# Kernel tuning notes

Measured on AMD Instinct MI355X. Metric: run time of the kernel, lower is better.

The kernel has to match this reference:

```python
import jax, jax.numpy as jnp
import numpy as np

B, T, I, H, O = 32, 2048, 128, 256, 64


def setup_inputs() -> dict:
    key = jax.random.key(0)
    ks = jax.random.split(key, 7)
    s = 0.05
    return {
        "x": jax.random.normal(ks[0], (B, T, I), dtype=jnp.float32),
        # PyTorch LSTM params (single layer): gate order i, f, g, o
        "W_ih": jax.random.normal(ks[1], (4 * H, I), dtype=jnp.float32) * s,
        "W_hh": jax.random.normal(ks[2], (4 * H, H), dtype=jnp.float32) * s,
        "b_ih": jax.random.normal(ks[3], (4 * H,), dtype=jnp.float32) * s,
        "b_hh": jax.random.normal(ks[4], (4 * H,), dtype=jnp.float32) * s,
        "W_fc": jax.random.normal(ks[5], (O, H), dtype=jnp.float32) * s,
        "b_fc": jax.random.normal(ks[6], (O,), dtype=jnp.float32) * s,
    }


def _lstm(x, W_ih, W_hh, b_ih, b_hh):
    # x: (B, T, I) -> hidden states (B, T, H). PyTorch gate order i,f,g,o.
    Bn, Tn, _ = x.shape
    Hn = W_hh.shape[1]
    # Precompute input projection once (memory-bound friendly):
    x_proj = jnp.einsum("bti,gi->btg", x, W_ih) + b_ih + b_hh  # (B, T, 4H)
    x_proj = jnp.swapaxes(x_proj, 0, 1)  # (T, B, 4H)

    def step(carry, xt):
        h, c = carry
        gates = xt + h @ W_hh.T  # (B, 4H)
        i, f, g, o = jnp.split(gates, 4, axis=-1)
        i = jax.nn.sigmoid(i)
        f = jax.nn.sigmoid(f)
        g = jnp.tanh(g)
        o = jax.nn.sigmoid(o)
        c = f * c + i * g
        h = o * jnp.tanh(c)
        return (h, c), h

    h0 = jnp.zeros((Bn, Hn), dtype=x.dtype)
    c0 = jnp.zeros((Bn, Hn), dtype=x.dtype)
    _, hs = jax.lax.scan(step, (h0, c0), x_proj)  # (T, B, H)
    return jnp.swapaxes(hs, 0, 1)  # (B, T, H)


def reference(x, W_ih, W_hh, b_ih, b_hh, W_fc, b_fc):
    h = _lstm(x, W_ih, W_hh, b_ih, b_hh)          # (B, T, H)
    logits = jnp.einsum("bth,oh->bto", h, W_fc) + b_fc  # fused fc over all (b,t)
    # original applies softmax over the feature vector at each (i, j)
    return jax.nn.softmax(logits, axis=-1)        # (B, T, O)
```

## Files before the change

kernel.cpp:

```cpp
#include <hip/hip_runtime.h>
#include <hip/hip_bf16.h>
#include <hip/hip_fp16.h>

typedef _Float16 v2h __attribute__((ext_vector_type(2)));

__device__ __forceinline__ float fdot2u(unsigned int a, unsigned int b, float c){
  return __builtin_amdgcn_fdot2(__builtin_bit_cast(v2h, a), __builtin_bit_cast(v2h, b), c, false);
}
__device__ __forceinline__ unsigned int packh2(float a, float b){
  union{ _Float16 h[2]; unsigned int u; } z;
  z.h[0] = (_Float16)a; z.h[1] = (_Float16)b; return z.u;
}
__device__ __forceinline__ float h2f(unsigned short s){
  return (float)__builtin_bit_cast(_Float16, s);
}
__device__ __forceinline__ float sigf(float x){
  return __builtin_amdgcn_rcpf(1.0f + __builtin_amdgcn_exp2f(-1.44269504f*x));
}
__device__ __forceinline__ float tanhf_(float x){
  return 2.0f*__builtin_amdgcn_rcpf(1.0f + __builtin_amdgcn_exp2f(-2.88539008f*x)) - 1.0f;
}

__global__ void prep_kernel(const float* __restrict__ Whh, const float* __restrict__ Wfc,
                            const float* __restrict__ bih, const float* __restrict__ bhh,
                            unsigned int* __restrict__ whhT, unsigned int* __restrict__ wfc16,
                            float* __restrict__ bsum){
  int i = blockIdx.x*256 + threadIdx.x;
  if (i < 131072){
    int r = i >> 7, d = i & 127;
    int q = d >> 2, l = d & 3;
    whhT[q*4096 + r*4 + l] = packh2(Whh[r*256 + 2*d], Whh[r*256 + 2*d + 1]);
  } else if (i < 139264){
    int j = i - 131072; int o = j >> 7, d = j & 127;
    wfc16[j] = packh2(Wfc[o*256 + 2*d], Wfc[o*256 + 2*d + 1]);
  } else if (i < 140288){
    int g = i - 139264;
    bsum[g] = bih[g] + bhh[g];
  }
}

#define XS 68
__global__ __launch_bounds__(256) void xproj_kernel(const float* __restrict__ x,
                          const float* __restrict__ Wih,
                          const float* __restrict__ bsum, unsigned int* __restrict__ xproj){
  __shared__ unsigned int lx[128*XS];
  __shared__ unsigned int lw[64*XS];
  __shared__ float lb[64];
  int t  = threadIdx.x;
  int bt0 = blockIdx.x*128, g0 = blockIdx.y*64;
  int rr = t >> 4, cc = t & 15;
  #pragma unroll
  for (int it=0; it<8; ++it){
    int row = rr + it*16;
    const float4* s = (const float4*)(x + (size_t)(bt0+row)*128 + cc*8);
    float4 a = s[0], b = s[1];
    uint4 w; w.x=packh2(a.x,a.y); w.y=packh2(a.z,a.w); w.z=packh2(b.x,b.y); w.w=packh2(b.z,b.w);
    *(uint4*)&lx[row*XS + cc*4] = w;
  }
  #pragma unroll
  for (int it=0; it<4; ++it){
    int row = rr + it*16;
    const float4* s = (const float4*)(Wih + (size_t)(g0+row)*128 + cc*8);
    float4 a = s[0], b = s[1];
    uint4 w; w.x=packh2(a.x,a.y); w.y=packh2(a.z,a.w); w.z=packh2(b.x,b.y); w.w=packh2(b.z,b.w);
    *(uint4*)&lw[row*XS + cc*4] = w;
  }
  if (t < 64) lb[t] = bsum[g0 + t];
  __syncthreads();

  float acc[8][4];
  #pragma unroll
  for (int j=0;j<8;++j)
    #pragma unroll
    for (int i=0;i<4;++i) acc[j][i]=0.f;

  #pragma unroll
  for (int d4=0; d4<16; ++d4){
    uint4 wv[4], xv[8];
    #pragma unroll
    for (int i=0;i<4;++i) wv[i] = *(const uint4*)&lw[(cc*4+i)*XS + d4*4];
    #pragma unroll
    for (int j=0;j<8;++j) xv[j] = *(const uint4*)&lx[(rr*8+j)*XS + d4*4];
    #pragma unroll
    for (int j=0;j<8;++j){
      #pragma unroll
      for (int i=0;i<4;++i){
        float a = acc[j][i];
        a = fdot2u(xv[j].x, wv[i].x, a);
        a = fdot2u(xv[j].y, wv[i].y, a);
        a = fdot2u(xv[j].z, wv[i].z, a);
        a = fdot2u(xv[j].w, wv[i].w, a);
        acc[j][i] = a;
      }
    }
  }
  #pragma unroll
  for (int j=0;j<8;++j){
    int bt = bt0 + rr*8 + j;
    uint2 o2;
    o2.x = packh2(acc[j][0]+lb[cc*4+0], acc[j][1]+lb[cc*4+1]);
    o2.y = packh2(acc[j][2]+lb[cc*4+2], acc[j][3]+lb[cc*4+3]);
    *(uint2*)&xproj[(size_t)bt*512 + (g0>>1) + cc*2] = o2;
  }
}

#define WR4 24
#define WL4 8
#define HOFF (WL4*4096)
#define GOFF (HOFF + 256)

extern "C" __global__ void __launch_bounds__(1024,4) lstm_kernel(
    const unsigned int* __restrict__ whhT, const unsigned int* __restrict__ xproj,
    unsigned short* __restrict__ h_all)
{
  extern __shared__ unsigned int lds[];
  uint4* lw4 = (uint4*)lds;
  float* gbuf = (float*)(lds + GOFF);
  const int t = threadIdx.x;
  const int g = t >> 8, u = t & 255;
  const int b = blockIdx.x;

  const uint4* wsrc = (const uint4*)whhT;
  uint4 w4[WR4];
  #pragma unroll
  for (int d=0; d<WR4; ++d) w4[d] = wsrc[d*1024 + t];
  #pragma unroll
  for (int q=0; q<WL4; ++q) lw4[q*1024 + t] = wsrc[(WR4+q)*1024 + t];
  if (t < 128) lds[HOFF + t] = 0u;

  const unsigned short* xpb = (const unsigned short*)xproj + (size_t)b*2048*1024;
  unsigned short xn = xpb[t];
  float c = 0.f;
  unsigned short* hout = h_all + (size_t)b*2048*256 + u;
  __syncthreads();

  for (int tt=0; tt<2048; ++tt){
    const int cur = tt & 1;
    float A0 = h2f(xn), A1 = 0.f;

    int tn = (tt+1 < 2048) ? tt+1 : 2047;
    xn = xpb[(size_t)tn*1024 + t];

    const unsigned int* hb = lds + HOFF + cur*128;
    #pragma unroll
    for (int d=0; d<WR4; ++d){
      uint4 h4 = *(const uint4*)(hb + d*4);
      A0 = fdot2u(w4[d].x, h4.x, A0); A1 = fdot2u(w4[d].y, h4.y, A1);
      A0 = fdot2u(w4[d].z, h4.z, A0); A1 = fdot2u(w4[d].w, h4.w, A1);
    }
    #pragma unroll
    for (int q=0; q<WL4; ++q){
      uint4 wl = lw4[q*1024 + t];
      uint4 h4 = *(const uint4*)(hb + (WR4+q)*4);
      A0 = fdot2u(wl.x, h4.x, A0); A1 = fdot2u(wl.y, h4.y, A1);
      A0 = fdot2u(wl.z, h4.z, A0); A1 = fdot2u(wl.w, h4.w, A1);
    }
    float a = A0 + A1;
    float v = (g == 2) ? tanhf_(a) : sigf(a);
    gbuf[g*256 + u] = v;
    __syncthreads();

    float gi = gbuf[u];
    float gf = gbuf[256 + u];
    float gg = gbuf[512 + u];
    float go = gbuf[768 + u];
    c = gf*c + gi*gg;
    float h = go * tanhf_(c);
    unsigned short hh = __builtin_bit_cast(unsigned short, (_Float16)h);
    if (g == 0){
      ((unsigned short*)(lds + HOFF + (cur^1)*128))[u] = hh;
      hout[(size_t)tt*256] = hh;
    }
    __syncthreads();
  }
}

__global__ __launch_bounds__(1024) void fc_softmax_kernel(const unsigned short* __restrict__ h_all,
      const unsigned int* __restrict__ wfc16, const float* __restrict__ bfc,
      float* __restrict__ out){
  __shared__ unsigned int lwf[64*132];
  __shared__ unsigned int lh[16*132];
  int t = threadIdx.x;
  int bt0 = blockIdx.x*16;
  {
    const uint4* s = (const uint4*)(wfc16 + (size_t)t*8);
    uint4 a = s[0], b = s[1];
    unsigned int* dst = &lwf[(t>>4)*132 + (t&15)*8];
    *(uint4*)dst = a; *(uint4*)(dst+4) = b;
  }
  {
    int row = t>>6, col = (t&63)*2;
    const unsigned int* hsrc = (const unsigned int*)h_all;
    uint2 v = *(const uint2*)(hsrc + (size_t)(bt0+row)*128 + col);
    *(uint2*)&lh[row*132 + col] = v;
  }
  __syncthreads();
  int w = t>>6, o = t&63;
  int bt = bt0 + w;
  float acc = bfc[o];
  #pragma unroll
  for (int d4=0; d4<32; ++d4){
    uint4 hq = *(const uint4*)&lh[w*132 + d4*4];
    uint4 wq = *(const uint4*)&lwf[o*132 + d4*4];
    acc = fdot2u(wq.x, hq.x, acc);
    acc = fdot2u(wq.y, hq.y, acc);
    acc = fdot2u(wq.z, hq.z, acc);
    acc = fdot2u(wq.w, hq.w, acc);
  }
  float m = acc;
  #pragma unroll
  for (int off=32; off>=1; off>>=1) m = fmaxf(m, __shfl_xor(m, off));
  float e = __builtin_amdgcn_exp2f(1.44269504f*(acc - m));
  float s = e;
  #pragma unroll
  for (int off=32; off>=1; off>>=1) s += __shfl_xor(s, off);
  out[(size_t)bt*64 + o] = e * __builtin_amdgcn_rcpf(s);
}

extern "C" void kernel_launch(void* const* d_in, const int* in_sizes, int n_in,
                              void* d_out, int out_size, void* d_ws, size_t ws_size,
                              hipStream_t stream){
  const float* x   = (const float*)d_in[0];
  const float* Wih = (const float*)d_in[1];
  const float* Whh = (const float*)d_in[2];
  const float* bih = (const float*)d_in[3];
  const float* bhh = (const float*)d_in[4];
  const float* Wfc = (const float*)d_in[5];
  const float* bfc = (const float*)d_in[6];
  float* out = (float*)d_out;

  char* ws = (char*)d_ws;
  unsigned int*   xproj = (unsigned int*)ws;
  unsigned short* h_all = (unsigned short*)(ws + 134217728);
  unsigned int*   whhT  = (unsigned int*)(ws + 134217728 + 33554432);
  unsigned int*   wfc16 = whhT + 131072;
  float*          bsum  = (float*)(wfc16 + 8192);

  prep_kernel<<<548, 256, 0, stream>>>(Whh, Wfc, bih, bhh, whhT, wfc16, bsum);
  dim3 gb(512, 16);
  xproj_kernel<<<gb, 256, 0, stream>>>(x, Wih, bsum, xproj);
  int dyn = (GOFF + 1024) * 4;
  hipFuncSetAttribute((const void*)lstm_kernel, hipFuncAttributeMaxDynamicSharedMemorySize, dyn);
  lstm_kernel<<<32, 1024, dyn, stream>>>(whhT, xproj, h_all);
  fc_softmax_kernel<<<4096, 1024, 0, stream>>>(h_all, wfc16, bfc, out);
}
```

Before: 3.457 ms.

## Split LSTM recurrence by hidden-dim quarter to drop one barrier per step

Each group of four consecutive threads now owns one hidden unit. Each thread holds all four gate rows over a quarter of the hidden dimension, so gate pre-activations are reduced with two xor shuffles instead of an LDS gate buffer and a second __syncthreads. The W_hh layout in prep is rearranged to match. Each thread also reads only its own padded slice of h, which cuts LDS broadcast reads. The cost is four transcendental gate evaluations per thread and replicated cell-state math, and all four lanes now write h to LDS.

```diff
diff --git a/kernel.cpp b/kernel.cpp
--- a/kernel.cpp
+++ b/kernel.cpp
@@ -23,13 +23,14 @@
 
 __global__ void prep_kernel(const float* __restrict__ Whh, const float* __restrict__ Wfc,
                             const float* __restrict__ bih, const float* __restrict__ bhh,
-                            unsigned int* __restrict__ whhT, unsigned int* __restrict__ wfc16,
+                            unsigned int* __restrict__ whhT2, unsigned int* __restrict__ wfc16,
                             float* __restrict__ bsum){
   int i = blockIdx.x*256 + threadIdx.x;
   if (i < 131072){
     int r = i >> 7, d = i & 127;
-    int q = d >> 2, l = d & 3;
-    whhT[q*4096 + r*4 + l] = packh2(Whh[r*256 + 2*d], Whh[r*256 + 2*d + 1]);
+    int g = r >> 8, u = r & 255;
+    int p = d >> 5, j = (d >> 2) & 7, l = d & 3;
+    whhT2[(size_t)((g*8+j)*1024 + u*4 + p)*4 + l] = packh2(Whh[r*256 + 2*d], Whh[r*256 + 2*d + 1]);
   } else if (i < 139264){
     int j = i - 131072; int o = j >> 7, d = j & 127;
     wfc16[j] = packh2(Wfc[o*256 + 2*d], Wfc[o*256 + 2*d + 1]);
@@ -104,73 +105,78 @@
   }
 }
 
-#define WR4 24
 #define WL4 8
 #define HOFF (WL4*4096)
-#define GOFF (HOFF + 256)
+#define HBUF 528
 
 extern "C" __global__ void __launch_bounds__(1024,4) lstm_kernel(
-    const unsigned int* __restrict__ whhT, const unsigned int* __restrict__ xproj,
+    const unsigned int* __restrict__ whhT2, const unsigned int* __restrict__ xproj,
     unsigned short* __restrict__ h_all)
 {
   extern __shared__ unsigned int lds[];
   uint4* lw4 = (uint4*)lds;
-  float* gbuf = (float*)(lds + GOFF);
+  unsigned short* lds16 = (unsigned short*)lds;
   const int t = threadIdx.x;
-  const int g = t >> 8, u = t & 255;
+  const int u = t >> 2, p = t & 3;
   const int b = blockIdx.x;
-
-  const uint4* wsrc = (const uint4*)whhT;
-  uint4 w4[WR4];
-  #pragma unroll
-  for (int d=0; d<WR4; ++d) w4[d] = wsrc[d*1024 + t];
-  #pragma unroll
-  for (int q=0; q<WL4; ++q) lw4[q*1024 + t] = wsrc[(WR4+q)*1024 + t];
-  if (t < 128) lds[HOFF + t] = 0u;
-
+  const int p164 = p*164;
+
+  const uint4* wsrc = (const uint4*)whhT2;
+  uint4 w4[3][8];
+  #pragma unroll
+  for (int g=0; g<3; ++g)
+    #pragma unroll
+    for (int j=0; j<8; ++j) w4[g][j] = wsrc[(g*8+j)*1024 + t];
+  #pragma unroll
+  for (int q=0; q<WL4; ++q) lw4[q*1024 + t] = wsrc[(24+q)*1024 + t];
+  if (t < HBUF) lds[HOFF + t] = 0u;
+
+  const float m0 = (p==0)?1.f:0.f, m1 = (p==1)?1.f:0.f,
+              m2 = (p==2)?1.f:0.f, m3 = (p==3)?1.f:0.f;
   const unsigned short* xpb = (const unsigned short*)xproj + (size_t)b*2048*1024;
-  unsigned short xn = xpb[t];
+  const int xoff = p*256 + u;
+  unsigned short xn = xpb[xoff];
   float c = 0.f;
   unsigned short* hout = h_all + (size_t)b*2048*256 + u;
   __syncthreads();
 
   for (int tt=0; tt<2048; ++tt){
     const int cur = tt & 1;
-    float A0 = h2f(xn), A1 = 0.f;
-
+    float A0 = 0.f, A1 = 0.f, A2 = 0.f, A3 = 0.f;
+    float xv = h2f(xn);
     int tn = (tt+1 < 2048) ? tt+1 : 2047;
-    xn = xpb[(size_t)tn*1024 + t];
-
-    const unsigned int* hb = lds + HOFF + cur*128;
-    #pragma unroll
-    for (int d=0; d<WR4; ++d){
-      uint4 h4 = *(const uint4*)(hb + d*4);
-      A0 = fdot2u(w4[d].x, h4.x, A0); A1 = fdot2u(w4[d].y, h4.y, A1);
-      A0 = fdot2u(w4[d].z, h4.z, A0); A1 = fdot2u(w4[d].w, h4.w, A1);
+    xn = xpb[(size_t)tn*1024 + xoff];
+
+    const unsigned int* hb = lds + HOFF + cur*HBUF + p164;
+    #pragma unroll
+    for (int j=0; j<8; ++j){
+      uint4 h4 = *(const uint4*)(hb + j*4);
+      uint4 wo = lw4[j*1024 + t];
+      A0 = fdot2u(w4[0][j].x, h4.x, A0); A0 = fdot2u(w4[0][j].y, h4.y, A0);
+      A0 = fdot2u(w4[0][j].z, h4.z, A0); A0 = fdot2u(w4[0][j].w, h4.w, A0);
+      A1 = fdot2u(w4[1][j].x, h4.x, A1); A1 = fdot2u(w4[1][j].y, h4.y, A1);
+      A1 = fdot2u(w4[1][j].z, h4.z, A1); A1 = fdot2u(w4[1][j].w, h4.w, A1);
+      A2 = fdot2u(w4[2][j].x, h4.x, A2); A2 = fdot2u(w4[2][j].y, h4.y, A2);
+      A2 = fdot2u(w4[2][j].z, h4.z, A2); A2 = fdot2u(w4[2][j].w, h4.w, A2);
+      A3 = fdot2u(wo.x, h4.x, A3); A3 = fdot2u(wo.y, h4.y, A3);
+      A3 = fdot2u(wo.z, h4.z, A3); A3 = fdot2u(wo.w, h4.w, A3);
     }
-    #pragma unroll
-    for (int q=0; q<WL4; ++q){
-      uint4 wl = lw4[q*1024 + t];
-      uint4 h4 = *(const uint4*)(hb + (WR4+q)*4);
-      A0 = fdot2u(wl.x, h4.x, A0); A1 = fdot2u(wl.y, h4.y, A1);
-      A0 = fdot2u(wl.z, h4.z, A0); A1 = fdot2u(wl.w, h4.w, A1);
-    }
-    float a = A0 + A1;
-    float v = (g == 2) ? tanhf_(a) : sigf(a);
-    gbuf[g*256 + u] = v;
-    __syncthreads();
-
-    float gi = gbuf[u];
-    float gf = gbuf[256 + u];
-    float gg = gbuf[512 + u];
-    float go = gbuf[768 + u];
+    A0 = fmaf(m0, xv, A0); A1 = fmaf(m1, xv, A1);
+    A2 = fmaf(m2, xv, A2); A3 = fmaf(m3, xv, A3);
+    A0 += __shfl_xor(A0, 1); A1 += __shfl_xor(A1, 1);
+    A2 += __shfl_xor(A2, 1); A3 += __shfl_xor(A3, 1);
+    A0 += __shfl_xor(A0, 2); A1 += __shfl_xor(A1, 2);
+    A2 += __shfl_xor(A2, 2); A3 += __shfl_xor(A3, 2);
+
+    float gi = sigf(A0);
+    float gf = sigf(A1);
+    float gg = tanhf_(A2);
+    float go = sigf(A3);
     c = gf*c + gi*gg;
     float h = go * tanhf_(c);
     unsigned short hh = __builtin_bit_cast(unsigned short, (_Float16)h);
-    if (g == 0){
-      ((unsigned short*)(lds + HOFF + (cur^1)*128))[u] = hh;
-      hout[(size_t)tt*256] = hh;
-    }
+    lds16[(HOFF + (cur^1)*HBUF + p*132)*2 + u] = hh;
+    if (p == 0) hout[(size_t)tt*256] = hh;
     __syncthreads();
   }
 }
@@ -232,15 +238,15 @@
   char* ws = (char*)d_ws;
   unsigned int*   xproj = (unsigned int*)ws;
   unsigned short* h_all = (unsigned short*)(ws + 134217728);
-  unsigned int*   whhT  = (unsigned int*)(ws + 134217728 + 33554432);
-  unsigned int*   wfc16 = whhT + 131072;
+  unsigned int*   whhT2 = (unsigned int*)(ws + 134217728 + 33554432);
+  unsigned int*   wfc16 = whhT2 + 131072;
   float*          bsum  = (float*)(wfc16 + 8192);
 
-  prep_kernel<<<548, 256, 0, stream>>>(Whh, Wfc, bih, bhh, whhT, wfc16, bsum);
+  prep_kernel<<<548, 256, 0, stream>>>(Whh, Wfc, bih, bhh, whhT2, wfc16, bsum);
   dim3 gb(512, 16);
   xproj_kernel<<<gb, 256, 0, stream>>>(x, Wih, bsum, xproj);
-  int dyn = (GOFF + 1024) * 4;
+  int dyn = (HOFF + 2*HBUF) * 4;
   hipFuncSetAttribute((const void*)lstm_kernel, hipFuncAttributeMaxDynamicSharedMemorySize, dyn);
-  lstm_kernel<<<32, 1024, dyn, stream>>>(whhT, xproj, h_all);
+  lstm_kernel<<<32, 1024, dyn, stream>>>(whhT2, xproj, h_all);
   fc_softmax_kernel<<<4096, 1024, 0, stream>>>(h_all, wfc16, bfc, out);
 }
```

Result: slower. 4.241 ms (+22.7%).

## Split LSTM recurrence across four workgroups per batch with global-flag sync

Applied to the files above, without the earlier changes.

The recurrent kernel now uses 128 workgroups of 512 threads instead of 32 of 1024. Each of the four workgroups per batch row handles one gate, and two threads split each row's dot product and combine it with a DPP lane swap. All W_hh weights now fit in registers, so the LDS-resident weight slice is gone. Gate activations are exchanged through global memory, with an atomic counter barrier between the four workgroups every timestep. This spreads the work over more compute units but adds a cross-workgroup global sync and a global round trip per step. It also relies on all 128 workgroups being co-resident.

```diff
diff --git a/kernel.cpp b/kernel.cpp
--- a/kernel.cpp
+++ b/kernel.cpp
@@ -20,22 +20,29 @@
 __device__ __forceinline__ float tanhf_(float x){
   return 2.0f*__builtin_amdgcn_rcpf(1.0f + __builtin_amdgcn_exp2f(-2.88539008f*x)) - 1.0f;
 }
+__device__ __forceinline__ float dpp_xor1(float x){
+  return __builtin_bit_cast(float,
+    __builtin_amdgcn_mov_dpp(__builtin_bit_cast(int, x), 0xB1, 0xF, 0xF, true));
+}
 
 __global__ void prep_kernel(const float* __restrict__ Whh, const float* __restrict__ Wfc,
                             const float* __restrict__ bih, const float* __restrict__ bhh,
-                            unsigned int* __restrict__ whhT, unsigned int* __restrict__ wfc16,
-                            float* __restrict__ bsum){
+                            unsigned int* __restrict__ whhT3, unsigned int* __restrict__ wfc16,
+                            float* __restrict__ bsum, unsigned int* __restrict__ flags){
   int i = blockIdx.x*256 + threadIdx.x;
   if (i < 131072){
     int r = i >> 7, d = i & 127;
-    int q = d >> 2, l = d & 3;
-    whhT[q*4096 + r*4 + l] = packh2(Whh[r*256 + 2*d], Whh[r*256 + 2*d + 1]);
+    int g = r >> 8, u = r & 255;
+    int p = (d >> 6) & 1, j = (d >> 2) & 15, l = d & 3;
+    whhT3[(size_t)((g*16+j)*512 + u*2 + p)*4 + l] = packh2(Whh[r*256 + 2*d], Whh[r*256 + 2*d + 1]);
   } else if (i < 139264){
     int j = i - 131072; int o = j >> 7, d = j & 127;
     wfc16[j] = packh2(Wfc[o*256 + 2*d], Wfc[o*256 + 2*d + 1]);
   } else if (i < 140288){
     int g = i - 139264;
     bsum[g] = bih[g] + bhh[g];
+  } else if (i < 140320){
+    flags[i - 140288] = 0u;
   }
 }
 
@@ -104,72 +111,76 @@
   }
 }
 
-#define WR4 24
-#define WL4 8
-#define HOFF (WL4*4096)
-#define GOFF (HOFF + 256)
-
-extern "C" __global__ void __launch_bounds__(1024,4) lstm_kernel(
-    const unsigned int* __restrict__ whhT, const unsigned int* __restrict__ xproj,
-    unsigned short* __restrict__ h_all)
+extern "C" __global__ void __launch_bounds__(512,2) lstm_kernel(
+    const unsigned int* __restrict__ whhT3, const unsigned int* __restrict__ xproj,
+    unsigned short* __restrict__ h_all, float* __restrict__ acts,
+    unsigned int* __restrict__ flags)
 {
-  extern __shared__ unsigned int lds[];
-  uint4* lw4 = (uint4*)lds;
-  float* gbuf = (float*)(lds + GOFF);
+  __shared__ unsigned int hlds[2][136];
   const int t = threadIdx.x;
-  const int g = t >> 8, u = t & 255;
-  const int b = blockIdx.x;
-
-  const uint4* wsrc = (const uint4*)whhT;
-  uint4 w4[WR4];
-  #pragma unroll
-  for (int d=0; d<WR4; ++d) w4[d] = wsrc[d*1024 + t];
-  #pragma unroll
-  for (int q=0; q<WL4; ++q) lw4[q*1024 + t] = wsrc[(WR4+q)*1024 + t];
-  if (t < 128) lds[HOFF + t] = 0u;
-
-  const unsigned short* xpb = (const unsigned short*)xproj + (size_t)b*2048*1024;
-  unsigned short xn = xpb[t];
+  const int u = t >> 1, p = t & 1;
+  const int wg = blockIdx.x;
+  const int b = wg & 31, gg = wg >> 5;
+
+  uint4 w4[16];
+  {
+    const uint4* wsrc = (const uint4*)whhT3;
+    #pragma unroll
+    for (int j=0; j<16; ++j) w4[j] = wsrc[(gg*16+j)*512 + t];
+  }
+  if (t < 136){ hlds[0][t] = 0u; hlds[1][t] = 0u; }
+
+  const unsigned short* xpb = (const unsigned short*)xproj
+                              + (size_t)b*2048*1024 + gg*256 + u;
+  unsigned short xn = xpb[0];
   float c = 0.f;
   unsigned short* hout = h_all + (size_t)b*2048*256 + u;
+  unsigned int* flg = flags + b;
   __syncthreads();
 
   for (int tt=0; tt<2048; ++tt){
     const int cur = tt & 1;
-    float A0 = h2f(xn), A1 = 0.f;
-
+    float xv = h2f(xn);
     int tn = (tt+1 < 2048) ? tt+1 : 2047;
-    xn = xpb[(size_t)tn*1024 + t];
-
-    const unsigned int* hb = lds + HOFF + cur*128;
-    #pragma unroll
-    for (int d=0; d<WR4; ++d){
-      uint4 h4 = *(const uint4*)(hb + d*4);
-      A0 = fdot2u(w4[d].x, h4.x, A0); A1 = fdot2u(w4[d].y, h4.y, A1);
-      A0 = fdot2u(w4[d].z, h4.z, A0); A1 = fdot2u(w4[d].w, h4.w, A1);
-    }
-    #pragma unroll
-    for (int q=0; q<WL4; ++q){
-      uint4 wl = lw4[q*1024 + t];
-      uint4 h4 = *(const uint4*)(hb + (WR4+q)*4);
-      A0 = fdot2u(wl.x, h4.x, A0); A1 = fdot2u(wl.y, h4.y, A1);
-      A0 = fdot2u(wl.z, h4.z, A0); A1 = fdot2u(wl.w, h4.w, A1);
-    }
-    float a = A0 + A1;
-    float v = (g == 2) ? tanhf_(a) : sigf(a);
-    gbuf[g*256 + u] = v;
+    xn = xpb[(size_t)tn*1024];
+
+    const unsigned int* hb = &hlds[cur][p*68];
+    float A0 = 0.f, A1 = 0.f;
+    #pragma unroll
+    for (int j=0; j<16; ++j){
+      uint4 h4 = *(const uint4*)(hb + j*4);
+      A0 = fdot2u(w4[j].x, h4.x, A0); A1 = fdot2u(w4[j].y, h4.y, A1);
+      A0 = fdot2u(w4[j].z, h4.z, A0); A1 = fdot2u(w4[j].w, h4.w, A1);
+    }
+    float A = A0 + A1;
+    A += dpp_xor1(A);
+    A += xv;
+    float act = (gg == 2) ? tanhf_(A) : sigf(A);
+
+    float* ab = acts + ((size_t)b*2 + cur)*1024;
+    if (p == 0) ab[gg*256 + u] = act;
     __syncthreads();
 
-    float gi = gbuf[u];
-    float gf = gbuf[256 + u];
-    float gg = gbuf[512 + u];
-    float go = gbuf[768 + u];
-    c = gf*c + gi*gg;
+    if (t == 0){
+      __hip_atomic_fetch_add(flg, 1u, __ATOMIC_RELEASE, __HIP_MEMORY_SCOPE_AGENT);
+      unsigned int target = 4u*(unsigned)(tt+1);
+      while (__hip_atomic_fetch_add(flg, 0u, __ATOMIC_ACQUIRE, __HIP_MEMORY_SCOPE_AGENT) < target){
+        __builtin_amdgcn_s_sleep(1);
+      }
+    }
+    __syncthreads();
+
+    const float* ar = acts + ((size_t)b*2 + cur)*1024;
+    float gi = ar[u];
+    float gf = ar[256 + u];
+    float g_ = ar[512 + u];
+    float go = ar[768 + u];
+    c = gf*c + gi*g_;
     float h = go * tanhf_(c);
     unsigned short hh = __builtin_bit_cast(unsigned short, (_Float16)h);
-    if (g == 0){
-      ((unsigned short*)(lds + HOFF + (cur^1)*128))[u] = hh;
-      hout[(size_t)tt*256] = hh;
+    if (p == 0){
+      ((unsigned short*)hlds[cur^1])[(u < 128) ? u : (u + 8)] = hh;
+      if (gg == 0) hout[(size_t)tt*256] = hh;
     }
     __syncthreads();
   }
@@ -232,15 +243,15 @@
   char* ws = (char*)d_ws;
   unsigned int*   xproj = (unsigned int*)ws;
   unsigned short* h_all = (unsigned short*)(ws + 134217728);
-  unsigned int*   whhT  = (unsigned int*)(ws + 134217728 + 33554432);
-  unsigned int*   wfc16 = whhT + 131072;
+  unsigned int*   whhT3 = (unsigned int*)(ws + 134217728 + 33554432);
+  unsigned int*   wfc16 = whhT3 + 131072;
   float*          bsum  = (float*)(wfc16 + 8192);
-
-  prep_kernel<<<548, 256, 0, stream>>>(Whh, Wfc, bih, bhh, whhT, wfc16, bsum);
+  unsigned int*   flags = (unsigned int*)(bsum + 1024);
+  float*          acts  = (float*)(flags + 32);
+
+  prep_kernel<<<549, 256, 0, stream>>>(Whh, Wfc, bih, bhh, whhT3, wfc16, bsum, flags);
   dim3 gb(512, 16);
   xproj_kernel<<<gb, 256, 0, stream>>>(x, Wih, bsum, xproj);
-  int dyn = (GOFF + 1024) * 4;
-  hipFuncSetAttribute((const void*)lstm_kernel, hipFuncAttributeMaxDynamicSharedMemorySize, dyn);
-  lstm_kernel<<<32, 1024, dyn, stream>>>(whhT, xproj, h_all);
+  lstm_kernel<<<128, 512, 0, stream>>>(whhT3, xproj, h_all, acts, flags);
   fc_softmax_kernel<<<4096, 1024, 0, stream>>>(h_all, wfc16, bfc, out);
 }
```

Result: slower. 9.687 ms (+180.2%).
